# Kernel tuning notes

Hardware: AMD Instinct MI355X
Metric: run time of the kernel (lower is better)

The kernel has to match this reference:

```python
import jax, jax.numpy as jnp
import numpy as np
from jax import lax

K = 3            # kernel size
KP = K * K       # kernel_size_prod
CENTER = KP // 2 # center tap index
PIXEL_SIZE = 1.0
DILATION = 1


def _unfold(x):
    # torch F.unfold equivalent: [N, C*KP, oh, ow] with channel-major, spatial-minor tap order
    return lax.conv_general_dilated_patches(
        x, filter_shape=(K, K), window_strides=(1, 1),
        padding=((1, 1), (1, 1)), rhs_dilation=(DILATION, DILATION))


def setup_inputs() -> dict:
    key = jax.random.key(0)
    ks = jax.random.split(key, 6)
    N, C, O, H, W = 8, 128, 128, 64, 64
    x = jax.random.normal(ks[0], (N, C, H, W), jnp.float32)
    depth = jax.random.uniform(ks[1], (N, 1, H, W), jnp.float32)  # >0 almost surely
    fx = jax.random.uniform(ks[2], (N,), jnp.float32) + 0.5       # per-image focal scale
    s = 1.0 / np.sqrt(C * KP)
    w0 = jax.random.normal(ks[3], (O, C, K, K), jnp.float32) * s
    w1 = jax.random.normal(ks[4], (O, C, K, K), jnp.float32) * s
    w2 = jax.random.normal(ks[5], (O, C, K, K), jnp.float32) * s
    return {"x": x, "depth": depth, "fx": fx, "w0": w0, "w1": w1, "w2": w2}


def reference(x, depth, fx, w0, w1, w2):
    N, C, H, W = x.shape
    O = w0.shape[0]
    patches = _unfold(x)                      # [N, C*9, oh, ow]
    oh, ow = patches.shape[2], patches.shape[3]
    L = oh * ow
    x_col = patches.reshape(N, C, KP, L)       # [N, C, 9, L]
    d_col = _unfold(depth).reshape(N, KP, L)   # [N, 9, L]

    valid = (d_col != 0.0).astype(jnp.float32)
    valid = valid * valid[:, CENTER:CENTER + 1, :]
    d_col = d_col * valid
    center = d_col[:, CENTER:CENTER + 1, :]    # [N, 1, L]
    grid = PIXEL_SIZE * DILATION * center / fx[:, None, None]
    half = grid * 0.5

    m0 = (jnp.abs(d_col - (center + grid)) <= half).astype(jnp.float32)
    m1 = (jnp.abs(d_col - center) <= half).astype(jnp.float32)
    m1 = jnp.clip(m1 + 1.0 - valid, 0.0, 1.0)
    m2 = (jnp.abs(d_col - (center - grid)) <= half).astype(jnp.float32)

    def branch(w, m):
        # (O, C*9) @ (N, C*9, L) as an einsum over (C, tap)
        return jnp.einsum('ock,nckl->nol', w.reshape(O, C, KP), x_col * m[:, None])

    out = branch(w0, m0) + branch(w1, m1) + branch(w2, m2)
    return out.reshape(N, O, oh, ow)
```

## Files before the change

### kernel.cpp

```cpp
#include <hip/hip_runtime.h>
#include <hip/hip_bf16.h>
#include <cstdint>
#include <cstddef>

#define Nn 8
#define Cc 128
#define Oo 128
#define Hh 64
#define Ww 64
#define LL (Hh * Ww)
#define KP 9

typedef __attribute__((ext_vector_type(8))) short short8;
typedef __attribute__((ext_vector_type(4))) float floatx4;
typedef __attribute__((ext_vector_type(16))) float f32x16;
typedef __attribute__((ext_vector_type(4))) int intx4;

#define SGB(m, s, i) __builtin_amdgcn_sched_group_barrier(m, s, i)

__device__ __forceinline__ unsigned short f2bf(float f) {
  unsigned int u = __float_as_uint(f);
  u += 0x7fffu + ((u >> 16) & 1u);
  return (unsigned short)(u >> 16);
}

__global__ __launch_bounds__(256) void prep_all(const float* __restrict__ x,
                                                const float* __restrict__ w0,
                                                const float* __restrict__ w1,
                                                const float* __restrict__ w2,
                                                const float* __restrict__ depth,
                                                const float* __restrict__ fx,
                                                unsigned short* __restrict__ xt,
                                                unsigned short* __restrict__ wt2,
                                                unsigned int* __restrict__ codesg) {
  __shared__ float tile[Cc][Ww + 1];
  __shared__ unsigned short wl[Cc * KP];
  const int bid = blockIdx.x;
  const int t = threadIdx.x;
  if (bid < Nn * Hh) {
    const int n = bid >> 6;
    const int h = bid & 63;
    const float* src = x + (size_t)n * Cc * LL + (size_t)h * Ww;
#pragma unroll
    for (int it = 0; it < 8; ++it) {
      const int idx = t + it * 256;
      const int c = idx >> 4;
      const int w4 = (idx & 15) << 2;
      const float4 v = *reinterpret_cast<const float4*>(src + (size_t)c * LL + w4);
      tile[c][w4 + 0] = v.x; tile[c][w4 + 1] = v.y;
      tile[c][w4 + 2] = v.z; tile[c][w4 + 3] = v.w;
    }
    __syncthreads();
    unsigned short* dst = xt + (size_t)((n * Hh + h) * Ww) * Cc;
#pragma unroll
    for (int it = 0; it < 4; ++it) {
      const int idx = t + it * 256;
      const int w = idx >> 4;
      const int ch = (idx & 15) << 3;
      short8 v;
#pragma unroll
      for (int q = 0; q < 8; ++q)
        ((unsigned short*)&v)[q] = f2bf(tile[ch + q][w]);
      *reinterpret_cast<short8*>(dst + (size_t)w * Cc + ch) = v;
    }
  } else if (bid < Nn * Hh + 3 * Oo) {
    const int bo = bid - Nn * Hh;
    const int b = bo >> 7;
    const int o = bo & 127;
    const float* w = (b == 0) ? w0 : (b == 1) ? w1 : w2;
    const float* src = w + (size_t)o * Cc * KP;
#pragma unroll
    for (int it = 0; it < 5; ++it) {
      const int idx = t + it * 256;
      if (idx < Cc * KP) wl[idx] = f2bf(src[idx]);
    }
    __syncthreads();
#pragma unroll
    for (int it = 0; it < 5; ++it) {
      const int idx = t + it * 256;
      if (idx < Cc * KP) {
        const int kk = idx >> 7;
        const int c = idx & 127;
        wt2[(size_t)(((b * 9 + kk) * 16 + (c >> 3)) * 128 + o) * 8 + (c & 7)] =
            wl[c * KP + kk];
      }
    }
  } else {
    const int p = (bid - (Nn * Hh + 3 * Oo)) * 256 + t;
    const int n = p >> 12;
    const int rem = p & 4095;
    const int h = rem >> 6;
    const int w = rem & 63;
    const float center = depth[p];
    const float grid = center / fx[n];
    const float half = 0.5f * grid;
    unsigned int packed = 0u;
#pragma unroll
    for (int kk = 0; kk < KP; ++kk) {
      const int hh = h + kk / 3 - 1;
      const int ww = w + kk % 3 - 1;
      float d = 0.0f;
      if (hh >= 0 && hh < Hh && ww >= 0 && ww < Ww) d = depth[(n << 12) + hh * Ww + ww];
      const float valid = (d != 0.0f && center != 0.0f) ? 1.0f : 0.0f;
      const float dm = d * valid;
      unsigned int cb = 0u;
      if (fabsf(dm - (center + grid)) <= half) cb |= 1u;
      float m1v = (fabsf(dm - center) <= half) ? 1.0f : 0.0f;
      m1v = m1v + 1.0f - valid;
      if (m1v > 1.0f) m1v = 1.0f;
      if (m1v > 0.5f) cb |= 2u;
      if (fabsf(dm - (center - grid)) <= half) cb |= 4u;
      packed |= cb << (3 * kk);
    }
    codesg[p] = packed;
  }
}

#define LDXC 132
#define HALO_COLS 66
#define HALO_ROWS 4
#define NSTEP 18

__global__ __launch_bounds__(256, 2) void conv_main(
    const unsigned short* __restrict__ xt,
    const unsigned short* __restrict__ wt2,
    const unsigned int* __restrict__ codesg,
    float* __restrict__ out) {
  __shared__ __align__(16) unsigned short Xs[HALO_ROWS * HALO_COLS * LDXC];

  const int g = blockIdx.x;
  const int n = g >> 6;
  const int rem = g & 63;
  const int pb = rem >> 1;
  const int ob1 = rem & 1;
  const int h0 = pb * 2;

  const int tid = threadIdx.x;
  const int lane = tid & 63;
  const int wave = tid >> 6;
  const int l31 = lane & 31;
  const int lg = lane >> 5;
  const int wc = wave & 1;
  const int ks = wave >> 1;

  const unsigned short* wf =
      wt2 + ((size_t)(ks * 8 + lg) * 128 + ob1 * 64 + wc * 32 + l31) * 8;

  short8 Bb[3][6];
  short8 Aa[2][8];

#define LOADB(SLOT, S)                                                               \
  {                                                                                  \
    const int kkq = (S) >> 1, hfq = (S) & 1;                                         \
    _Pragma("unroll")                                                                \
    for (int kc = 0; kc < 2; ++kc)                                                   \
      _Pragma("unroll")                                                              \
      for (int b = 0; b < 3; ++b)                                                    \
        Bb[SLOT][kc * 3 + b] = *reinterpret_cast<const short8*>(                     \
            wf + (size_t)(((b * 9 + kkq) * 16 + hfq * 4 + kc * 2)) * 1024);          \
  }

#define LOADA(SLOT, S)                                                               \
  {                                                                                  \
    const int kkp = (S) >> 1, hfp = (S) & 1;                                         \
    const int dyp = kkp / 3, dxp = kkp % 3;                                          \
    _Pragma("unroll")                                                                \
    for (int mt = 0; mt < 4; ++mt)                                                   \
      _Pragma("unroll")                                                              \
      for (int kc = 0; kc < 2; ++kc) {                                               \
        const int pix = ((mt >> 1) + dyp) * HALO_COLS + (mt & 1) * 32 + l31 + dxp;   \
        const int coff = ks * 64 + hfp * 32 + kc * 16 + lg * 8;                      \
        Aa[SLOT][mt * 2 + kc] =                                                      \
            *reinterpret_cast<const short8*>(&Xs[pix * LDXC + coff]);                \
      }                                                                              \
  }

  LOADB(0, 0)
  LOADB(1, 1)

  unsigned int cd2[4];
  {
    const unsigned int* cp = codesg + (n << 12) + h0 * 64;
#pragma unroll
    for (int mt = 0; mt < 4; ++mt) cd2[mt] = cp[mt * 32 + l31];
  }

#pragma unroll
  for (int it = 0; it < 17; ++it) {
    const int idx = tid + it * 256;
    if (idx < HALO_ROWS * HALO_COLS * 16) {
      const int ch = (idx & 15) << 3;
      const int pixidx = idx >> 4;
      const int lc = pixidx % HALO_COLS;
      const int hrel = pixidx / HALO_COLS;
      const int hh = h0 - 1 + hrel;
      const int ww = lc - 1;
      short8 v = {0, 0, 0, 0, 0, 0, 0, 0};
      if (hh >= 0 && hh < Hh && ww >= 0 && ww < Ww)
        v = *reinterpret_cast<const short8*>(
            xt + (size_t)((n * Hh + hh) * Ww + ww) * Cc + ch);
      *reinterpret_cast<short8*>(&Xs[pixidx * LDXC + ch]) = v;
    }
  }

  __syncthreads();

  f32x16 acc2[4];
#pragma unroll
  for (int mt = 0; mt < 4; ++mt)
    acc2[mt] = (f32x16){0.f, 0.f, 0.f, 0.f, 0.f, 0.f, 0.f, 0.f,
                        0.f, 0.f, 0.f, 0.f, 0.f, 0.f, 0.f, 0.f};

  LOADA(0, 0)

#pragma unroll
  for (int s = 0; s < NSTEP; ++s) {
    if (s + 2 < NSTEP) LOADB((s + 2) % 3, s + 2)
    if (s + 1 < NSTEP) LOADA((s + 1) & 1, s + 1)
    const int kk = s >> 1;
    const int shift = 3 * kk;
    const short8* B = Bb[s % 3];
    const short8* A = Aa[s & 1];
#pragma unroll
    for (int b = 0; b < 3; ++b) {
      int msk[4];
#pragma unroll
      for (int mt = 0; mt < 4; ++mt)
        msk[mt] = __builtin_amdgcn_sbfe((int)cd2[mt], shift + b, 1);
#pragma unroll
      for (int kc = 0; kc < 2; ++kc) {
#pragma unroll
        for (int mt = 0; mt < 4; ++mt) {
          intx4 a4 = *reinterpret_cast<const intx4*>(&A[mt * 2 + kc]);
          intx4 m4 = {msk[mt], msk[mt], msk[mt], msk[mt]};
          a4 &= m4;
          const short8 af = *reinterpret_cast<const short8*>(&a4);
          acc2[mt] = __builtin_amdgcn_mfma_f32_32x32x16_bf16(af, B[kc * 3 + b],
                                                             acc2[mt], 0, 0, 0);
        }
      }
    }
    SGB(0x020, 1, 0); SGB(0x008, 2, 0); SGB(0x100, 1, 0); SGB(0x008, 2, 0);
    SGB(0x020, 1, 0); SGB(0x008, 2, 0); SGB(0x100, 1, 0); SGB(0x008, 2, 0);
    SGB(0x020, 1, 0); SGB(0x008, 2, 0); SGB(0x100, 1, 0); SGB(0x008, 2, 0);
    SGB(0x020, 1, 0); SGB(0x008, 2, 0); SGB(0x100, 1, 0); SGB(0x008, 2, 0);
    SGB(0x020, 1, 0); SGB(0x008, 2, 0); SGB(0x100, 1, 0); SGB(0x008, 2, 0);
    SGB(0x020, 1, 0); SGB(0x008, 2, 0); SGB(0x100, 3, 0); SGB(0x008, 2, 0);
  }

  __syncthreads();
  float* scratch = reinterpret_cast<float*>(Xs);
  if (ks == 1) {
#pragma unroll
    for (int mt = 0; mt < 4; ++mt)
#pragma unroll
      for (int q4 = 0; q4 < 4; ++q4) {
        const floatx4 v = {acc2[mt][q4 * 4 + 0], acc2[mt][q4 * 4 + 1],
                           acc2[mt][q4 * 4 + 2], acc2[mt][q4 * 4 + 3]};
        *reinterpret_cast<floatx4*>(
            &scratch[(((wc * 4 + mt) * 4 + q4) * 64 + lane) * 4]) = v;
      }
  }
  __syncthreads();
  if (ks == 0) {
    const int o = ob1 * 64 + wc * 32 + l31;
#pragma unroll
    for (int mt = 0; mt < 4; ++mt) {
      const int h = h0 + (mt >> 1);
      const int wbase = (mt & 1) * 32;
#pragma unroll
      for (int q4 = 0; q4 < 4; ++q4) {
        const floatx4 other = *reinterpret_cast<const floatx4*>(
            &scratch[(((wc * 4 + mt) * 4 + q4) * 64 + lane) * 4]);
        const floatx4 mine = {acc2[mt][q4 * 4 + 0], acc2[mt][q4 * 4 + 1],
                              acc2[mt][q4 * 4 + 2], acc2[mt][q4 * 4 + 3]};
        const floatx4 sum = mine + other;
        const int w = wbase + q4 * 8 + lg * 4;
        float* dst = out + (size_t)(n * Oo + o) * LL + h * Ww + w;
        *reinterpret_cast<floatx4*>(dst) = sum;
      }
    }
  }
}

extern "C" void kernel_launch(void* const* d_in, const int* in_sizes, int n_in,
                              void* d_out, int out_size, void* d_ws, size_t ws_size,
                              hipStream_t stream) {
  const float* x     = (const float*)d_in[0];
  const float* depth = (const float*)d_in[1];
  const float* fx    = (const float*)d_in[2];
  const float* w0    = (const float*)d_in[3];
  const float* w1    = (const float*)d_in[4];
  const float* w2    = (const float*)d_in[5];
  float* out = (float*)d_out;

  unsigned short* xt = (unsigned short*)d_ws;
  unsigned short* wt2 = xt + (size_t)Nn * Hh * Ww * Cc;
  unsigned int* codesg = (unsigned int*)(wt2 + (size_t)3 * KP * Oo * Cc);

  prep_all<<<Nn * Hh + 3 * Oo + 128, 256, 0, stream>>>(x, w0, w1, w2, depth, fx, xt, wt2, codesg);
  conv_main<<<512, 256, 0, stream>>>(xt, wt2, codesg, out);
}
```

Before: 110.4 us.

## Replace fully unrolled 18-step loop with rolled 8-iteration double-buffered pipeline

Turns the fully unrolled 18-step MFMA loop into a rolled loop of 8 iterations, each covering two half-steps, followed by a peeled final tap. The weight register buffer shrinks from triple to double buffering, with B loads issued after each compute instead of two steps ahead. The sched_group_barrier pattern is rewritten to interleave VALU mask ops, MFMAs, global loads and LDS reads differently. The aim is smaller code, lower register pressure and better instruction interleaving, at the cost of a shorter prefetch distance for global weight loads and some runtime index arithmetic.

```diff
diff --git a/kernel.cpp b/kernel.cpp
--- a/kernel.cpp
+++ b/kernel.cpp
@@ -119,7 +119,6 @@
 #define LDXC 132
 #define HALO_COLS 66
 #define HALO_ROWS 4
-#define NSTEP 18
 
 __global__ __launch_bounds__(256, 2) void conv_main(
     const unsigned short* __restrict__ xt,
@@ -146,12 +145,12 @@
   const unsigned short* wf =
       wt2 + ((size_t)(ks * 8 + lg) * 128 + ob1 * 64 + wc * 32 + l31) * 8;
 
-  short8 Bb[3][6];
+  short8 Bb[2][6];
   short8 Aa[2][8];
 
-#define LOADB(SLOT, S)                                                               \
+#define LOADB(SLOT, KK, HF)                                                          \
   {                                                                                  \
-    const int kkq = (S) >> 1, hfq = (S) & 1;                                         \
+    const int kkq = (KK), hfq = (HF);                                                \
     _Pragma("unroll")                                                                \
     for (int kc = 0; kc < 2; ++kc)                                                   \
       _Pragma("unroll")                                                              \
@@ -160,23 +159,62 @@
             wf + (size_t)(((b * 9 + kkq) * 16 + hfq * 4 + kc * 2)) * 1024);          \
   }
 
-#define LOADA(SLOT, S)                                                               \
+#define LOADA(SLOT, KK, HF)                                                          \
   {                                                                                  \
-    const int kkp = (S) >> 1, hfp = (S) & 1;                                         \
-    const int dyp = kkp / 3, dxp = kkp % 3;                                          \
+    const int kkp = (KK), hfp = (HF);                                                \
+    const int dyp = kkp / 3, dxp = kkp - dyp * 3;                                    \
+    const int pof = dyp * HALO_COLS + dxp + l31;                                     \
     _Pragma("unroll")                                                                \
     for (int mt = 0; mt < 4; ++mt)                                                   \
       _Pragma("unroll")                                                              \
       for (int kc = 0; kc < 2; ++kc) {                                               \
-        const int pix = ((mt >> 1) + dyp) * HALO_COLS + (mt & 1) * 32 + l31 + dxp;   \
+        const int pix = (mt >> 1) * HALO_COLS + (mt & 1) * 32 + pof;                 \
         const int coff = ks * 64 + hfp * 32 + kc * 16 + lg * 8;                      \
         Aa[SLOT][mt * 2 + kc] =                                                      \
             *reinterpret_cast<const short8*>(&Xs[pix * LDXC + coff]);                \
       }                                                                              \
   }
 
-  LOADB(0, 0)
-  LOADB(1, 1)
+#define COMPUTE(BSLOT, ASLOT, KK)                                                    \
+  {                                                                                  \
+    const int shift = 3 * (KK);                                                      \
+    _Pragma("unroll")                                                                \
+    for (int b = 0; b < 3; ++b) {                                                    \
+      int msk[4];                                                                    \
+      _Pragma("unroll")                                                              \
+      for (int mt = 0; mt < 4; ++mt)                                                 \
+        msk[mt] = __builtin_amdgcn_sbfe((int)cd2[mt], shift + b, 1);                 \
+      _Pragma("unroll")                                                              \
+      for (int kc = 0; kc < 2; ++kc) {                                               \
+        _Pragma("unroll")                                                            \
+        for (int mt = 0; mt < 4; ++mt) {                                             \
+          intx4 a4 = *reinterpret_cast<const intx4*>(&Aa[ASLOT][mt * 2 + kc]);       \
+          intx4 m4 = {msk[mt], msk[mt], msk[mt], msk[mt]};                           \
+          a4 &= m4;                                                                  \
+          const short8 af = *reinterpret_cast<const short8*>(&a4);                   \
+          acc2[mt] = __builtin_amdgcn_mfma_f32_32x32x16_bf16(                        \
+              af, Bb[BSLOT][kc * 3 + b], acc2[mt], 0, 0, 0);                         \
+        }                                                                            \
+      }                                                                              \
+    }                                                                                \
+  }
+
+#define STEP_SGB                                                                     \
+  SGB(0x008, 2, 0); SGB(0x100, 1, 0); SGB(0x020, 1, 0); SGB(0x002, 9, 0);            \
+  SGB(0x008, 2, 0); SGB(0x100, 1, 0); SGB(0x020, 1, 0); SGB(0x002, 9, 0);            \
+  SGB(0x008, 2, 0); SGB(0x100, 1, 0); SGB(0x020, 1, 0); SGB(0x002, 9, 0);            \
+  SGB(0x008, 2, 0); SGB(0x100, 1, 0); SGB(0x020, 1, 0); SGB(0x002, 9, 0);            \
+  SGB(0x008, 2, 0); SGB(0x100, 1, 0); SGB(0x020, 1, 0); SGB(0x002, 9, 0);            \
+  SGB(0x008, 2, 0); SGB(0x100, 1, 0); SGB(0x020, 1, 0); SGB(0x002, 9, 0);            \
+  SGB(0x008, 2, 0); SGB(0x100, 1, 0); SGB(0x002, 9, 0);                              \
+  SGB(0x008, 2, 0); SGB(0x100, 1, 0); SGB(0x002, 9, 0);                              \
+  SGB(0x008, 2, 0); SGB(0x002, 9, 0);                                                \
+  SGB(0x008, 2, 0); SGB(0x002, 9, 0);                                                \
+  SGB(0x008, 2, 0); SGB(0x002, 9, 0);                                                \
+  SGB(0x008, 2, 0); SGB(0x002, 9, 0);
+
+  LOADB(0, 0, 0)
+  LOADB(1, 0, 1)
 
   unsigned int cd2[4];
   {
@@ -211,42 +249,22 @@
     acc2[mt] = (f32x16){0.f, 0.f, 0.f, 0.f, 0.f, 0.f, 0.f, 0.f,
                         0.f, 0.f, 0.f, 0.f, 0.f, 0.f, 0.f, 0.f};
 
-  LOADA(0, 0)
-
-#pragma unroll
-  for (int s = 0; s < NSTEP; ++s) {
-    if (s + 2 < NSTEP) LOADB((s + 2) % 3, s + 2)
-    if (s + 1 < NSTEP) LOADA((s + 1) & 1, s + 1)
-    const int kk = s >> 1;
-    const int shift = 3 * kk;
-    const short8* B = Bb[s % 3];
-    const short8* A = Aa[s & 1];
-#pragma unroll
-    for (int b = 0; b < 3; ++b) {
-      int msk[4];
-#pragma unroll
-      for (int mt = 0; mt < 4; ++mt)
-        msk[mt] = __builtin_amdgcn_sbfe((int)cd2[mt], shift + b, 1);
-#pragma unroll
-      for (int kc = 0; kc < 2; ++kc) {
-#pragma unroll
-        for (int mt = 0; mt < 4; ++mt) {
-          intx4 a4 = *reinterpret_cast<const intx4*>(&A[mt * 2 + kc]);
-          intx4 m4 = {msk[mt], msk[mt], msk[mt], msk[mt]};
-          a4 &= m4;
-          const short8 af = *reinterpret_cast<const short8*>(&a4);
-          acc2[mt] = __builtin_amdgcn_mfma_f32_32x32x16_bf16(af, B[kc * 3 + b],
-                                                             acc2[mt], 0, 0, 0);
-        }
-      }
-    }
-    SGB(0x020, 1, 0); SGB(0x008, 2, 0); SGB(0x100, 1, 0); SGB(0x008, 2, 0);
-    SGB(0x020, 1, 0); SGB(0x008, 2, 0); SGB(0x100, 1, 0); SGB(0x008, 2, 0);
-    SGB(0x020, 1, 0); SGB(0x008, 2, 0); SGB(0x100, 1, 0); SGB(0x008, 2, 0);
-    SGB(0x020, 1, 0); SGB(0x008, 2, 0); SGB(0x100, 1, 0); SGB(0x008, 2, 0);
-    SGB(0x020, 1, 0); SGB(0x008, 2, 0); SGB(0x100, 1, 0); SGB(0x008, 2, 0);
-    SGB(0x020, 1, 0); SGB(0x008, 2, 0); SGB(0x100, 3, 0); SGB(0x008, 2, 0);
-  }
+  LOADA(0, 0, 0)
+
+#pragma unroll 1
+  for (int p = 0; p < 8; ++p) {
+    LOADA(1, p, 1)
+    COMPUTE(0, 0, p)
+    LOADB(0, p + 1, 0)
+    STEP_SGB
+    LOADA(0, p + 1, 0)
+    COMPUTE(1, 1, p)
+    LOADB(1, p + 1, 1)
+    STEP_SGB
+  }
+  LOADA(1, 8, 1)
+  COMPUTE(0, 0, 8)
+  COMPUTE(1, 1, 8)
 
   __syncthreads();
   float* scratch = reinterpret_cast<float*>(Xs);
```

Measured after the change: 111.9 us. No clear change (+1.4%).
